# Kernel optimization log

Hardware: AMD Instinct MI355X
Metric: run time of the kernel (lower is better)

The kernel has to match this reference:

```python
import jax, jax.numpy as jnp
import numpy as np

N, D = 8192, 128
EPS = 1.1920929e-07  # torch.finfo(float32).eps, nn.RMSNorm default when eps=None


def setup_inputs() -> dict:
    key = jax.random.key(0)
    k1, k2, k3, k4, k5 = jax.random.split(key, 5)
    x = jax.random.normal(k1, (N, D), dtype=jnp.float32)
    past_mem = jax.random.normal(k2, (N, D, D), dtype=jnp.float32)
    gamma = jnp.ones((D,), dtype=jnp.float32)  # RMSNorm elementwise affine weight
    w_qkv = jax.random.normal(k3, (3 * D, D), dtype=jnp.float32) * (1.0 / np.sqrt(D))
    w_forget = jax.random.normal(k4, (1, D), dtype=jnp.float32) * (1.0 / np.sqrt(D))
    return {"x": x, "past_mem": past_mem, "gamma": gamma, "w_qkv": w_qkv, "w_forget": w_forget}


def reference(x, past_mem, gamma, w_qkv, w_forget):
    # RMSNorm
    xn = x * jax.lax.rsqrt(jnp.mean(x * x, axis=-1, keepdims=True) + EPS) * gamma
    # QKV projection (no bias)
    qkv = xn @ w_qkv.T                      # [N, 3D]
    q, k, v = jnp.split(qkv, 3, axis=-1)    # each [N, D]
    q = jax.nn.silu(q)
    k = jax.nn.silu(k)
    # outer-product memory update: new_mem[n, d, e] = k[n, d] * v[n, e]
    new_mem = k[..., :, None] * v[..., None, :]      # [N, D, D]
    # per-token scalar forget gate
    forget = jax.nn.sigmoid(xn @ w_forget.T)         # [N, 1]
    f = forget[..., None]                            # [N, 1, 1]
    mem = past_mem + f * (new_mem - past_mem)        # lerp(past_mem, new_mem, forget)
    # retrieval: matvec against memory
    retrieved = jnp.einsum('nd,nde->ne', q, mem)     # [N, D]
    return retrieved, mem
```

## Files before the change

kernel.cpp:

```cpp
#include <hip/hip_runtime.h>
#include <math.h>

#define NROWS 8192
#define DD 128
#define EPSV 1.1920929e-07f

__global__ void __launch_bounds__(256)
fused_linattn(const float* __restrict__ x,
              const float* __restrict__ past_mem,
              const float* __restrict__ gamma,
              const float* __restrict__ w_qkv,
              const float* __restrict__ w_forget,
              float* __restrict__ out_retr,
              float* __restrict__ out_mem) {
    const int n = blockIdx.x;
    const int t = threadIdx.x;

    __shared__ __align__(16) float s_xn[DD];
    __shared__ __align__(16) float s_q[DD];
    __shared__ __align__(16) float s_k[DD];
    __shared__ __align__(16) float s_v[DD];
    __shared__ float s_tmp[4];
    __shared__ float4 s_red[256];

    float xv = 0.0f;
    if (t < DD) xv = x[(size_t)n * DD + t];
    float ss = xv * xv;
    #pragma unroll
    for (int off = 32; off > 0; off >>= 1) ss += __shfl_down(ss, off, 64);
    if ((t & 63) == 0) s_tmp[t >> 6] = ss;
    __syncthreads();
    const float sumsq = s_tmp[0] + s_tmp[1] + s_tmp[2] + s_tmp[3];
    const float rinv = rsqrtf(sumsq * (1.0f / DD) + EPSV);
    if (t < DD) s_xn[t] = xv * rinv * gamma[t];
    __syncthreads();

    float fp = (t < DD) ? s_xn[t] * w_forget[t] : 0.0f;
    #pragma unroll
    for (int off = 32; off > 0; off >>= 1) fp += __shfl_down(fp, off, 64);
    if ((t & 63) == 0) s_tmp[t >> 6] = fp;

    const float4* xn4 = (const float4*)s_xn;
    {
        const float4* wrow = (const float4*)(w_qkv + (size_t)t * DD);
        float a = 0.0f;
        #pragma unroll 8
        for (int i = 0; i < DD / 4; ++i) {
            float4 w4 = wrow[i];
            float4 xx = xn4[i];
            a = fmaf(w4.x, xx.x, a);
            a = fmaf(w4.y, xx.y, a);
            a = fmaf(w4.z, xx.z, a);
            a = fmaf(w4.w, xx.w, a);
        }
        const float s = a / (1.0f + expf(-a));
        if (t < DD) s_q[t] = s;
        else        s_k[t - DD] = s;
    }
    if (t < DD) {
        const float4* wrow = (const float4*)(w_qkv + (size_t)(t + 2 * DD) * DD);
        float a = 0.0f;
        #pragma unroll 8
        for (int i = 0; i < DD / 4; ++i) {
            float4 w4 = wrow[i];
            float4 xx = xn4[i];
            a = fmaf(w4.x, xx.x, a);
            a = fmaf(w4.y, xx.y, a);
            a = fmaf(w4.z, xx.z, a);
            a = fmaf(w4.w, xx.w, a);
        }
        s_v[t] = a;
    }
    __syncthreads();
    const float fdot = s_tmp[0] + s_tmp[1] + s_tmp[2] + s_tmp[3];
    const float f = 1.0f / (1.0f + expf(-fdot));

    const int qc = t & 31;
    const int dg = t >> 5;
    const float4 v4 = ((const float4*)s_v)[qc];
    float4 acc = make_float4(0.0f, 0.0f, 0.0f, 0.0f);
    const size_t base = (size_t)n * (DD * DD);
    const float4* past4 = (const float4*)(past_mem + base);
    float4* mem4 = (float4*)(out_mem + base);
    #pragma unroll 4
    for (int d = dg; d < DD; d += 8) {
        const float kd = s_k[d];
        const float qd = s_q[d];
        float4 p = past4[d * 32 + qc];
        float4 m;
        m.x = fmaf(f, fmaf(kd, v4.x, -p.x), p.x);
        m.y = fmaf(f, fmaf(kd, v4.y, -p.y), p.y);
        m.z = fmaf(f, fmaf(kd, v4.z, -p.z), p.z);
        m.w = fmaf(f, fmaf(kd, v4.w, -p.w), p.w);
        mem4[d * 32 + qc] = m;
        acc.x = fmaf(qd, m.x, acc.x);
        acc.y = fmaf(qd, m.y, acc.y);
        acc.z = fmaf(qd, m.z, acc.z);
        acc.w = fmaf(qd, m.w, acc.w);
    }
    s_red[t] = acc;
    __syncthreads();
    if (t < 32) {
        float4 tot = s_red[t];
        #pragma unroll
        for (int g = 1; g < 8; ++g) {
            float4 r = s_red[g * 32 + t];
            tot.x += r.x; tot.y += r.y; tot.z += r.z; tot.w += r.w;
        }
        ((float4*)(out_retr + (size_t)n * DD))[t] = tot;
    }
}

extern "C" void kernel_launch(void* const* d_in, const int* in_sizes, int n_in,
                              void* d_out, int out_size, void* d_ws, size_t ws_size,
                              hipStream_t stream) {
    (void)in_sizes; (void)n_in; (void)out_size; (void)d_ws; (void)ws_size;
    const float* x        = (const float*)d_in[0];
    const float* past_mem = (const float*)d_in[1];
    const float* gamma    = (const float*)d_in[2];
    const float* w_qkv    = (const float*)d_in[3];
    const float* w_forget = (const float*)d_in[4];
    float* out_retr = (float*)d_out;
    float* out_mem  = (float*)d_out + (size_t)NROWS * DD;

    fused_linattn<<<dim3(NROWS), dim3(256), 0, stream>>>(
        x, past_mem, gamma, w_qkv, w_forget, out_retr, out_mem);
}
```

Baseline: 939.4 us.

## Split QKV projection into row-batched kernel and stream memory update with nontemporal access

Moves RMSNorm, QKV projection and forget gate into a separate kernel that processes 16 rows per block, reusing each weight load across rows instead of re-reading the full weight matrix per token. Results are staged in the output memory buffer, then read back by a streaming kernel that performs the lerp and retrieval. The streaming kernel uses nontemporal loads and stores with deeper unrolling. This adds a kernel launch and a small round-trip through global memory.

After: 876.1 us. 1.07x faster.

```diff
diff --git a/kernel.cpp b/kernel.cpp
--- a/kernel.cpp
+++ b/kernel.cpp
@@ -4,100 +4,147 @@
 #define NROWS 8192
 #define DD 128
 #define EPSV 1.1920929e-07f
+#define ROWS 16
+
+typedef float v4f __attribute__((ext_vector_type(4)));
+
+__device__ __forceinline__ float sigmoidf_(float a) { return 1.0f / (1.0f + expf(-a)); }
+
+__global__ void __launch_bounds__(128)
+qkvf_kernel(const float* __restrict__ x,
+            const float* __restrict__ gamma,
+            const float* __restrict__ w_qkv,
+            const float* __restrict__ w_forget,
+            float* __restrict__ out_mem) {
+    const int t = threadIdx.x;
+    const int rb = blockIdx.x * ROWS;
+
+    __shared__ __align__(16) float s_xn[ROWS][DD];
+    __shared__ float s_f[ROWS];
+
+    {
+        const int r = t >> 3;
+        const int l = t & 7;
+        const float4* xr = (const float4*)(x + (size_t)(rb + r) * DD);
+        float4 xa[4];
+        #pragma unroll
+        for (int j = 0; j < 4; ++j) xa[j] = xr[l * 4 + j];
+        float ss = 0.0f;
+        #pragma unroll
+        for (int j = 0; j < 4; ++j)
+            ss += xa[j].x * xa[j].x + xa[j].y * xa[j].y +
+                  xa[j].z * xa[j].z + xa[j].w * xa[j].w;
+        #pragma unroll
+        for (int off = 1; off < 8; off <<= 1) ss += __shfl_xor(ss, off, 64);
+        const float rinv = rsqrtf(ss * (1.0f / DD) + EPSV);
+
+        float fp = 0.0f;
+        #pragma unroll
+        for (int j = 0; j < 4; ++j) {
+            const float4 g  = ((const float4*)gamma)[l * 4 + j];
+            const float4 wf = ((const float4*)w_forget)[l * 4 + j];
+            float4 xn;
+            xn.x = xa[j].x * rinv * g.x;
+            xn.y = xa[j].y * rinv * g.y;
+            xn.z = xa[j].z * rinv * g.z;
+            xn.w = xa[j].w * rinv * g.w;
+            fp += xn.x * wf.x + xn.y * wf.y + xn.z * wf.z + xn.w * wf.w;
+            ((float4*)s_xn[r])[l * 4 + j] = xn;
+        }
+        #pragma unroll
+        for (int off = 1; off < 8; off <<= 1) fp += __shfl_xor(fp, off, 64);
+        if (l == 0) s_f[r] = sigmoidf_(fp);
+    }
+    __syncthreads();
+
+    float accq[ROWS], acck[ROWS], accv[ROWS];
+    #pragma unroll
+    for (int r = 0; r < ROWS; ++r) { accq[r] = 0.f; acck[r] = 0.f; accv[r] = 0.f; }
+    const float4* wq = (const float4*)(w_qkv + (size_t)t * DD);
+    const float4* wk = (const float4*)(w_qkv + (size_t)(t + DD) * DD);
+    const float4* wv = (const float4*)(w_qkv + (size_t)(t + 2 * DD) * DD);
+    #pragma unroll 2
+    for (int i = 0; i < DD / 4; ++i) {
+        const float4 a = wq[i];
+        const float4 b = wk[i];
+        const float4 c = wv[i];
+        #pragma unroll
+        for (int r = 0; r < ROWS; ++r) {
+            const float4 xx = ((const float4*)s_xn[r])[i];
+            accq[r] = fmaf(a.x, xx.x, accq[r]);
+            accq[r] = fmaf(a.y, xx.y, accq[r]);
+            accq[r] = fmaf(a.z, xx.z, accq[r]);
+            accq[r] = fmaf(a.w, xx.w, accq[r]);
+            acck[r] = fmaf(b.x, xx.x, acck[r]);
+            acck[r] = fmaf(b.y, xx.y, acck[r]);
+            acck[r] = fmaf(b.z, xx.z, acck[r]);
+            acck[r] = fmaf(b.w, xx.w, acck[r]);
+            accv[r] = fmaf(c.x, xx.x, accv[r]);
+            accv[r] = fmaf(c.y, xx.y, accv[r]);
+            accv[r] = fmaf(c.z, xx.z, accv[r]);
+            accv[r] = fmaf(c.w, xx.w, accv[r]);
+        }
+    }
+    #pragma unroll
+    for (int r = 0; r < ROWS; ++r) {
+        float* st = out_mem + (size_t)(rb + r) * (DD * DD);
+        st[t]          = accq[r] * sigmoidf_(accq[r]);
+        st[DD + t]     = acck[r] * sigmoidf_(acck[r]);
+        st[2 * DD + t] = accv[r];
+    }
+    if (t < ROWS) out_mem[(size_t)(rb + t) * (DD * DD) + 3 * DD] = s_f[t];
+}
 
 __global__ void __launch_bounds__(256)
-fused_linattn(const float* __restrict__ x,
-              const float* __restrict__ past_mem,
-              const float* __restrict__ gamma,
-              const float* __restrict__ w_qkv,
-              const float* __restrict__ w_forget,
+stream_kernel(const float* __restrict__ past_mem,
               float* __restrict__ out_retr,
               float* __restrict__ out_mem) {
     const int n = blockIdx.x;
     const int t = threadIdx.x;
 
-    __shared__ __align__(16) float s_xn[DD];
     __shared__ __align__(16) float s_q[DD];
     __shared__ __align__(16) float s_k[DD];
     __shared__ __align__(16) float s_v[DD];
-    __shared__ float s_tmp[4];
+    __shared__ float s_fv;
     __shared__ float4 s_red[256];
 
-    float xv = 0.0f;
-    if (t < DD) xv = x[(size_t)n * DD + t];
-    float ss = xv * xv;
-    #pragma unroll
-    for (int off = 32; off > 0; off >>= 1) ss += __shfl_down(ss, off, 64);
-    if ((t & 63) == 0) s_tmp[t >> 6] = ss;
-    __syncthreads();
-    const float sumsq = s_tmp[0] + s_tmp[1] + s_tmp[2] + s_tmp[3];
-    const float rinv = rsqrtf(sumsq * (1.0f / DD) + EPSV);
-    if (t < DD) s_xn[t] = xv * rinv * gamma[t];
+    const size_t base = (size_t)n * (DD * DD);
+    const float* stage = out_mem + base;
+
+    if (t < 96) {
+        const float4 val = ((const float4*)stage)[t];
+        if (t < 32)      ((float4*)s_q)[t]      = val;
+        else if (t < 64) ((float4*)s_k)[t - 32] = val;
+        else             ((float4*)s_v)[t - 64] = val;
+    }
+    if (t == 96) s_fv = stage[3 * DD];
     __syncthreads();
 
-    float fp = (t < DD) ? s_xn[t] * w_forget[t] : 0.0f;
-    #pragma unroll
-    for (int off = 32; off > 0; off >>= 1) fp += __shfl_down(fp, off, 64);
-    if ((t & 63) == 0) s_tmp[t >> 6] = fp;
-
-    const float4* xn4 = (const float4*)s_xn;
-    {
-        const float4* wrow = (const float4*)(w_qkv + (size_t)t * DD);
-        float a = 0.0f;
-        #pragma unroll 8
-        for (int i = 0; i < DD / 4; ++i) {
-            float4 w4 = wrow[i];
-            float4 xx = xn4[i];
-            a = fmaf(w4.x, xx.x, a);
-            a = fmaf(w4.y, xx.y, a);
-            a = fmaf(w4.z, xx.z, a);
-            a = fmaf(w4.w, xx.w, a);
-        }
-        const float s = a / (1.0f + expf(-a));
-        if (t < DD) s_q[t] = s;
-        else        s_k[t - DD] = s;
-    }
-    if (t < DD) {
-        const float4* wrow = (const float4*)(w_qkv + (size_t)(t + 2 * DD) * DD);
-        float a = 0.0f;
-        #pragma unroll 8
-        for (int i = 0; i < DD / 4; ++i) {
-            float4 w4 = wrow[i];
-            float4 xx = xn4[i];
-            a = fmaf(w4.x, xx.x, a);
-            a = fmaf(w4.y, xx.y, a);
-            a = fmaf(w4.z, xx.z, a);
-            a = fmaf(w4.w, xx.w, a);
-        }
-        s_v[t] = a;
-    }
-    __syncthreads();
-    const float fdot = s_tmp[0] + s_tmp[1] + s_tmp[2] + s_tmp[3];
-    const float f = 1.0f / (1.0f + expf(-fdot));
-
+    const float f = s_fv;
     const int qc = t & 31;
     const int dg = t >> 5;
     const float4 v4 = ((const float4*)s_v)[qc];
     float4 acc = make_float4(0.0f, 0.0f, 0.0f, 0.0f);
-    const size_t base = (size_t)n * (DD * DD);
-    const float4* past4 = (const float4*)(past_mem + base);
-    float4* mem4 = (float4*)(out_mem + base);
-    #pragma unroll 4
+    const v4f* past4 = (const v4f*)(past_mem + base);
+    v4f* mem4 = (v4f*)(out_mem + base);
+
+    #pragma unroll 8
     for (int d = dg; d < DD; d += 8) {
         const float kd = s_k[d];
         const float qd = s_q[d];
-        float4 p = past4[d * 32 + qc];
-        float4 m;
+        const v4f p = __builtin_nontemporal_load(past4 + d * 32 + qc);
+        v4f m;
         m.x = fmaf(f, fmaf(kd, v4.x, -p.x), p.x);
         m.y = fmaf(f, fmaf(kd, v4.y, -p.y), p.y);
         m.z = fmaf(f, fmaf(kd, v4.z, -p.z), p.z);
         m.w = fmaf(f, fmaf(kd, v4.w, -p.w), p.w);
-        mem4[d * 32 + qc] = m;
+        __builtin_nontemporal_store(m, mem4 + d * 32 + qc);
         acc.x = fmaf(qd, m.x, acc.x);
         acc.y = fmaf(qd, m.y, acc.y);
         acc.z = fmaf(qd, m.z, acc.z);
         acc.w = fmaf(qd, m.w, acc.w);
     }
+
     s_red[t] = acc;
     __syncthreads();
     if (t < 32) {
@@ -123,6 +170,8 @@
     float* out_retr = (float*)d_out;
     float* out_mem  = (float*)d_out + (size_t)NROWS * DD;
 
-    fused_linattn<<<dim3(NROWS), dim3(256), 0, stream>>>(
-        x, past_mem, gamma, w_qkv, w_forget, out_retr, out_mem);
+    qkvf_kernel<<<dim3(NROWS / ROWS), dim3(128), 0, stream>>>(
+        x, gamma, w_qkv, w_forget, out_mem);
+    stream_kernel<<<dim3(NROWS), dim3(256), 0, stream>>>(
+        past_mem, out_retr, out_mem);
 }
```
